# Performance work log

Measured on AMD Instinct MI355X. Metric: run time of the kernel, lower is better.

## Reference

```python
import jax, jax.numpy as jnp
import numpy as np

B, L = 256, 8192
ACF_PAD = L - 1          # acf_class[1]
POOL = 8                 # acf_class[2]
ACF_SIZE = ACF_PAD + 1   # == L, length kept after trim
POOLED = ACF_SIZE // POOL  # 1024, MLP input size
LIN = [512, 256]
OUT = 4                  # no_reg=False -> 4 outputs


def _linear_init(key, fan_out, fan_in):
    kw, kb = jax.random.split(key)
    bound = 1.0 / np.sqrt(fan_in)
    W = jax.random.uniform(kw, (fan_out, fan_in), jnp.float32, -bound, bound)
    b = jax.random.uniform(kb, (fan_out,), jnp.float32, -bound, bound)
    return W, b


def setup_inputs() -> dict:
    key = jax.random.key(0)
    kx, k1, k2, k3 = jax.random.split(key, 4)
    x = jax.random.normal(kx, (B, 1, L), jnp.float32)
    W1, b1 = _linear_init(k1, LIN[0], POOLED)
    W2, b2 = _linear_init(k2, LIN[1], LIN[0])
    W3, b3 = _linear_init(k3, OUT, LIN[1])
    return {"x": x, "W1": W1, "b1": b1, "W2": W2, "b2": b2, "W3": W3, "b3": b3}


def reference(x, W1, b1, W2, b2, W3, b3):
    # x: [B, 1, L]. Grouped conv1d with groups=B == per-sample autocorrelation.
    a = x[:, 0, :]                                             # [B, L]
    # full cross-correlation of a with itself: [B, 2L-1], lags -(L-1)..(L-1)
    corr = jax.vmap(lambda v: jnp.correlate(v, v, mode="full"))(a)
    # trim [:, acf_pad:] keeps non-negative lags 0..L-1 -> length ACF_SIZE
    r = corr[:, L - 1:]                                        # [B, L]
    # MaxPool1d(POOL), stride == POOL, floor division (L divisible here)
    pooled = r.reshape(B, POOLED, POOL).max(axis=-1)           # [B, POOLED]
    # normalize by per-sample max
    norm = pooled / jnp.max(pooled, axis=1, keepdims=True)
    # MLP: (Dropout is identity at inference) Linear -> LeakyReLU x2 -> Linear
    h = jax.nn.leaky_relu(norm @ W1.T + b1, negative_slope=0.01)
    h = jax.nn.leaky_relu(h @ W2.T + b2, negative_slope=0.01)
    return h @ W3.T + b3                                       # [B, 4]
```

## Files before the change

### kernel.cpp

```cpp
#include <hip/hip_runtime.h>

typedef __attribute__((ext_vector_type(8))) short bf16x8;
typedef __attribute__((ext_vector_type(16))) float f32x16;

#define LN 8192
#define SA_ROWB 4240
#define SB_OFF  33920
#define SMEM_BYTES 65536

__device__ __forceinline__ unsigned short f2bf(float f) {
    unsigned int u = __float_as_uint(f);
    u += 0x7fffu + ((u >> 16) & 1u);
    return (unsigned short)(u >> 16);
}
__device__ __forceinline__ float lrelu(float v) { return v > 0.f ? v : 0.01f * v; }
__device__ __forceinline__ float gldx(const float* p, int i) { return (i >= 0 && i < LN) ? p[i] : 0.f; }

__device__ __forceinline__ void dot8bf(uint4 q, const float* nl, float& acc) {
    acc += __uint_as_float(q.x << 16)          * nl[0];
    acc += __uint_as_float(q.x & 0xffff0000u)  * nl[1];
    acc += __uint_as_float(q.y << 16)          * nl[2];
    acc += __uint_as_float(q.y & 0xffff0000u)  * nl[3];
    acc += __uint_as_float(q.z << 16)          * nl[4];
    acc += __uint_as_float(q.z & 0xffff0000u)  * nl[5];
    acc += __uint_as_float(q.w << 16)          * nl[6];
    acc += __uint_as_float(q.w & 0xffff0000u)  * nl[7];
}

__global__ __launch_bounds__(512)
void conv_kernel(const float* __restrict__ W1, unsigned short* __restrict__ W1bf)
{
    const int idx = blockIdx.x * 512 + threadIdx.x;
    float4 v = ((const float4*)W1)[idx];
    ushort4 o;
    o.x = f2bf(v.x); o.y = f2bf(v.y); o.z = f2bf(v.z); o.w = f2bf(v.w);
    ((ushort4*)W1bf)[idx] = o;
}

__global__ __launch_bounds__(1024)
void fused_kernel(const float* __restrict__ x,
                  const unsigned short* __restrict__ W1bf, const float* __restrict__ b1,
                  const float* __restrict__ W2, const float* __restrict__ b2,
                  const float* __restrict__ W3, const float* __restrict__ b3,
                  float* __restrict__ out)
{
    __shared__ __align__(16) unsigned char smem[SMEM_BYTES];
    __shared__ float red[16];

    const int tid  = threadIdx.x;
    const int row  = blockIdx.x;
    const int lane = tid & 63;
    const int wv   = tid >> 6;
    const float* xr = x + (size_t)row * LN;

    const int jj = lane & 31;
    const int gp = lane >> 5;
    const int dd = lane & 7;
    const int hh = (lane >> 3) & 3;
    const int aoff_lane = dd * SA_ROWB + 64 + 16 * gp - 16 * hh;

    const int q  = wv & 3;
    const int p  = wv >> 2;
    const int T1 = p;
    const int T2 = 7 - p;
    const int s1 = 512 - 64 * p;
    const int s2 = 64 + 64 * p;

    for (int s = tid; s < 1156; s += 1024) {
        const int e0 = s * 8;
        float4 fa, fb;
        if (e0 + 7 < LN) {
            fa = *(const float4*)(xr + e0);
            fb = *(const float4*)(xr + e0 + 4);
        } else {
            fa = make_float4(gldx(xr,e0),   gldx(xr,e0+1), gldx(xr,e0+2), gldx(xr,e0+3));
            fb = make_float4(gldx(xr,e0+4), gldx(xr,e0+5), gldx(xr,e0+6), gldx(xr,e0+7));
        }
        uint4 pk;
        pk.x = (unsigned)f2bf(fa.x) | ((unsigned)f2bf(fa.y) << 16);
        pk.y = (unsigned)f2bf(fa.z) | ((unsigned)f2bf(fa.w) << 16);
        pk.z = (unsigned)f2bf(fb.x) | ((unsigned)f2bf(fb.y) << 16);
        pk.w = (unsigned)f2bf(fb.z) | ((unsigned)f2bf(fb.w) << 16);
        const int ph = s ^ ((s >> 3) & 7);
        *(uint4*)(smem + SB_OFF + ph * 16) = pk;
    }

    f32x16 acc1 = {}, acc2 = {};

    for (int ch = 0; ch < 4; ++ch) {
        const int tc = ch << 11;
        __syncthreads();
        if (tid < 528) {
            const int base = tc + 4 * tid - 40;
            float4 fa, fb, fc;
            if (base >= 0 && base + 11 < LN) {
                fa = *(const float4*)(xr + base);
                fb = *(const float4*)(xr + base + 4);
                fc = *(const float4*)(xr + base + 8);
            } else {
                fa = make_float4(gldx(xr,base),   gldx(xr,base+1), gldx(xr,base+2),  gldx(xr,base+3));
                fb = make_float4(gldx(xr,base+4), gldx(xr,base+5), gldx(xr,base+6),  gldx(xr,base+7));
                fc = make_float4(gldx(xr,base+8), gldx(xr,base+9), gldx(xr,base+10), gldx(xr,base+11));
            }
            unsigned short us[12];
            us[0]=f2bf(fa.x); us[1]=f2bf(fa.y); us[2]=f2bf(fa.z);  us[3]=f2bf(fa.w);
            us[4]=f2bf(fb.x); us[5]=f2bf(fb.y); us[6]=f2bf(fb.z);  us[7]=f2bf(fb.w);
            us[8]=f2bf(fc.x); us[9]=f2bf(fc.y); us[10]=f2bf(fc.z); us[11]=f2bf(fc.w);
            #pragma unroll
            for (int d = 0; d < 8; ++d) {
                unsigned long long pk = (unsigned long long)us[8-d]
                                      | ((unsigned long long)us[9-d]  << 16)
                                      | ((unsigned long long)us[10-d] << 32)
                                      | ((unsigned long long)us[11-d] << 48);
                *(unsigned long long*)(smem + d * SA_ROWB + 8 * tid) = pk;
            }
        }
        __syncthreads();

        const int c0 = ch * 128;
        int dD = s2 - c0; dD = dD < 0 ? 0 : (dD > 128 ? 128 : dD);
        int sLo = c0 > s2 ? c0 : s2;
        int sHi = (c0 + 128) < s1 ? (c0 + 128) : s1;
        int sS = sHi - sLo; if (sS < 0) sS = 0;
        const int wd0 = c0 + q * (dD >> 2),  wd1 = c0 + (q + 1) * (dD >> 2);
        const int ws0 = sLo + q * (sS >> 2), ws1 = sLo + (q + 1) * (sS >> 2);

        {
            const unsigned char* ap = smem + aoff_lane + 32 * (wd0 - c0);
            int S1 = 128 * T1 + 2 * wd0 + 4 * jj + gp;
            int S2 = 128 * T2 + 2 * wd0 + 4 * jj + gp;
            for (int mq = wd0; mq < wd1; mq += 4) {
                bf16x8 A[4], B1[4], B2[4];
                #pragma unroll
                for (int u = 0; u < 4; ++u) {
                    A[u] = *(const bf16x8*)(ap + 32 * u);
                    const int sa = S1 + 2 * u, sb = S2 + 2 * u;
                    B1[u] = *(const bf16x8*)(smem + SB_OFF + ((sa ^ ((sa >> 3) & 7)) << 4));
                    B2[u] = *(const bf16x8*)(smem + SB_OFF + ((sb ^ ((sb >> 3) & 7)) << 4));
                }
                #pragma unroll
                for (int u = 0; u < 4; ++u) {
                    acc1 = __builtin_amdgcn_mfma_f32_32x32x16_bf16(A[u], B1[u], acc1, 0, 0, 0);
                    acc2 = __builtin_amdgcn_mfma_f32_32x32x16_bf16(A[u], B2[u], acc2, 0, 0, 0);
                }
                ap += 128; S1 += 8; S2 += 8;
            }
        }
        {
            const unsigned char* ap = smem + aoff_lane + 32 * (ws0 - c0);
            int S1 = 128 * T1 + 2 * ws0 + 4 * jj + gp;
            for (int mq = ws0; mq < ws1; mq += 4) {
                bf16x8 A[4], B1[4];
                #pragma unroll
                for (int u = 0; u < 4; ++u) {
                    A[u] = *(const bf16x8*)(ap + 32 * u);
                    const int sa = S1 + 2 * u;
                    B1[u] = *(const bf16x8*)(smem + SB_OFF + ((sa ^ ((sa >> 3) & 7)) << 4));
                }
                #pragma unroll
                for (int u = 0; u < 4; ++u)
                    acc1 = __builtin_amdgcn_mfma_f32_32x32x16_bf16(A[u], B1[u], acc1, 0, 0, 0);
                ap += 128; S1 += 8;
            }
        }
    }

    __syncthreads();

    auto pwrite = [&](int T, int s, const f32x16& acc, bool add) {
        unsigned char* bp = smem + (T * 2 + s) * 4096 + jj * 128;
        #pragma unroll
        for (int rq = 0; rq < 4; ++rq) {
            const int bi = (2 * rq + gp) ^ (jj & 7);
            float4 w = make_float4(acc[4*rq], acc[4*rq+1], acc[4*rq+2], acc[4*rq+3]);
            float4* pp = (float4*)(bp + bi * 16);
            if (add) { float4 o = *pp; w.x += o.x; w.y += o.y; w.z += o.z; w.w += o.w; }
            *pp = w;
        }
    };
    if (q < 2) { pwrite(T1, q, acc1, false); pwrite(T2, q, acc2, false); }
    __syncthreads();
    if (q >= 2) { pwrite(T1, q - 2, acc1, true); pwrite(T2, q - 2, acc2, true); }
    __syncthreads();

    float* nrm = (float*)smem;
    float* h1  = (float*)(smem + 4096);
    float* h2  = (float*)(smem + 6144);
    {
        const int T  = tid >> 7;
        const int j2 = (tid >> 2) & 31;
        const int rq = tid & 3;
        const unsigned char* b0 = smem + (T * 2) * 4096 + j2 * 128;
        const int biA = (2 * rq)     ^ (j2 & 7);
        const int biB = (2 * rq + 1) ^ (j2 & 7);
        float4 s0a = *(const float4*)(b0 + biA * 16);
        float4 s0b = *(const float4*)(b0 + biB * 16);
        float4 s1a = *(const float4*)(b0 + 4096 + biA * 16);
        float4 s1b = *(const float4*)(b0 + 4096 + biB * 16);
        float v0 = s0a.x + s1a.x, v1 = s0a.y + s1a.y, v2 = s0a.z + s1a.z, v3 = s0a.w + s1a.w;
        float v4 = s0b.x + s1b.x, v5 = s0b.y + s1b.y, v6 = s0b.z + s1b.z, v7 = s0b.w + s1b.w;
        float m = fmaxf(fmaxf(fmaxf(v0, v1), fmaxf(v2, v3)), fmaxf(fmaxf(v4, v5), fmaxf(v6, v7)));

        float mx = m;
        for (int off = 32; off > 0; off >>= 1) mx = fmaxf(mx, __shfl_xor(mx, off));
        if (lane == 0) red[wv] = mx;
        __syncthreads();
        float pmax = red[0];
        #pragma unroll
        for (int k = 1; k < 16; ++k) pmax = fmaxf(pmax, red[k]);
        nrm[tid] = m * (1.0f / pmax);
    }
    __syncthreads();

    {
        float nlo[8], nhi[8];
        {
            const float4* n4 = (const float4*)nrm;
            float4 a0 = n4[2 * lane], a1 = n4[2 * lane + 1];
            float4 b0 = n4[128 + 2 * lane], b1v = n4[128 + 2 * lane + 1];
            nlo[0]=a0.x; nlo[1]=a0.y; nlo[2]=a0.z; nlo[3]=a0.w;
            nlo[4]=a1.x; nlo[5]=a1.y; nlo[6]=a1.z; nlo[7]=a1.w;
            nhi[0]=b0.x; nhi[1]=b0.y; nhi[2]=b0.z; nhi[3]=b0.w;
            nhi[4]=b1v.x; nhi[5]=b1v.y; nhi[6]=b1v.z; nhi[7]=b1v.w;
        }
        for (int n0 = 0; n0 < 32; n0 += 4) {
            const int nb = wv * 32 + n0;
            float s0 = 0.f, s1 = 0.f, s2v = 0.f, s3 = 0.f;
            {
                const uint4* r0 = (const uint4*)(W1bf + (size_t)nb * 1024);
                const uint4* r1 = (const uint4*)(W1bf + (size_t)(nb + 1) * 1024);
                const uint4* r2 = (const uint4*)(W1bf + (size_t)(nb + 2) * 1024);
                const uint4* r3 = (const uint4*)(W1bf + (size_t)(nb + 3) * 1024);
                uint4 qa0 = r0[lane], qb0 = r0[64 + lane];
                uint4 qa1 = r1[lane], qb1 = r1[64 + lane];
                uint4 qa2 = r2[lane], qb2 = r2[64 + lane];
                uint4 qa3 = r3[lane], qb3 = r3[64 + lane];
                dot8bf(qa0, nlo, s0); dot8bf(qb0, nhi, s0);
                dot8bf(qa1, nlo, s1); dot8bf(qb1, nhi, s1);
                dot8bf(qa2, nlo, s2v); dot8bf(qb2, nhi, s2v);
                dot8bf(qa3, nlo, s3); dot8bf(qb3, nhi, s3);
            }
            #pragma unroll
            for (int off = 32; off > 0; off >>= 1) {
                s0 += __shfl_xor(s0, off);
                s1 += __shfl_xor(s1, off);
                s2v += __shfl_xor(s2v, off);
                s3 += __shfl_xor(s3, off);
            }
            if (lane == 0) {
                h1[nb]     = lrelu(s0 + b1[nb]);
                h1[nb + 1] = lrelu(s1 + b1[nb + 1]);
                h1[nb + 2] = lrelu(s2v + b1[nb + 2]);
                h1[nb + 3] = lrelu(s3 + b1[nb + 3]);
            }
        }
    }
    __syncthreads();

    {
        const float4* a4 = (const float4*)h1;
        float4 av0 = a4[lane], av1 = a4[lane + 64];
        #pragma unroll
        for (int n0 = 0; n0 < 16; n0 += 8) {
            const int nb = wv * 16 + n0;
            float s[8];
            #pragma unroll
            for (int u = 0; u < 8; ++u) {
                const float4* wr = (const float4*)(W2 + (size_t)(nb + u) * 512);
                float4 w0 = wr[lane], w1 = wr[lane + 64];
                float t0 = w0.x*av0.x + w0.y*av0.y + w0.z*av0.z + w0.w*av0.w;
                float t1 = w1.x*av1.x + w1.y*av1.y + w1.z*av1.z + w1.w*av1.w;
                s[u] = t0 + t1;
            }
            #pragma unroll
            for (int off = 32; off > 0; off >>= 1) {
                #pragma unroll
                for (int u = 0; u < 8; ++u) s[u] += __shfl_xor(s[u], off);
            }
            if (lane == 0) {
                #pragma unroll
                for (int u = 0; u < 8; ++u) h2[nb + u] = lrelu(s[u] + b2[nb + u]);
            }
        }
    }
    __syncthreads();

    if (wv < 4) {
        const float4 w = ((const float4*)(W3 + wv * 256))[lane];
        const float4 a = ((const float4*)h2)[lane];
        float s = w.x*a.x + w.y*a.y + w.z*a.z + w.w*a.w;
        for (int off = 32; off > 0; off >>= 1) s += __shfl_xor(s, off);
        if (lane == 0) out[row * 4 + wv] = s + b3[wv];
    }
}

extern "C" void kernel_launch(void* const* d_in, const int* in_sizes, int n_in,
                              void* d_out, int out_size, void* d_ws, size_t ws_size,
                              hipStream_t stream)
{
    const float* x  = (const float*)d_in[0];
    const float* W1 = (const float*)d_in[1];
    const float* b1 = (const float*)d_in[2];
    const float* W2 = (const float*)d_in[3];
    const float* b2 = (const float*)d_in[4];
    const float* W3 = (const float*)d_in[5];
    const float* b3 = (const float*)d_in[6];
    float* outp = (float*)d_out;
    unsigned short* W1bf = (unsigned short*)d_ws;

    hipLaunchKernelGGL(conv_kernel,  dim3(256), dim3(512),  0, stream, W1, W1bf);
    hipLaunchKernelGGL(fused_kernel, dim3(256), dim3(1024), 0, stream,
                       x, W1bf, b1, W2, b2, W3, b3, outp);
}
```

Baseline: 49.84 us.

## Transpose and pack MLP weights for thread-per-output dot products without shuffles

The preprocessing kernel now converts W1 and also W2 to bf16 and stores them k-major, in 8-element packs interleaved across output neurons. In the MLP layers each thread then computes one output neuron over a slice of K, using coalesced weight loads and broadcast activation reads from shared memory. This replaces the per-warp cross-lane shuffle reductions with small shared-memory partial-sum combines. W2 now runs in bf16, which adds rounding error, and the layer-1 loop is longer per thread, which may expose load latency.

Result: faster. 45.48 us, median of 2 (-8.8%).

```diff
diff --git a/kernel.cpp b/kernel.cpp
--- a/kernel.cpp
+++ b/kernel.cpp
@@ -26,21 +26,37 @@
     acc += __uint_as_float(q.w << 16)          * nl[6];
     acc += __uint_as_float(q.w & 0xffff0000u)  * nl[7];
 }
-
-__global__ __launch_bounds__(512)
-void conv_kernel(const float* __restrict__ W1, unsigned short* __restrict__ W1bf)
+__device__ __forceinline__ uint4 pack8(float4 a, float4 b) {
+    uint4 pk;
+    pk.x = (unsigned)f2bf(a.x) | ((unsigned)f2bf(a.y) << 16);
+    pk.y = (unsigned)f2bf(a.z) | ((unsigned)f2bf(a.w) << 16);
+    pk.z = (unsigned)f2bf(b.x) | ((unsigned)f2bf(b.y) << 16);
+    pk.w = (unsigned)f2bf(b.z) | ((unsigned)f2bf(b.w) << 16);
+    return pk;
+}
+
+__global__ __launch_bounds__(256)
+void conv_kernel(const float* __restrict__ W1, const float* __restrict__ W2,
+                 uint4* __restrict__ W1p, uint4* __restrict__ W2p)
 {
-    const int idx = blockIdx.x * 512 + threadIdx.x;
-    float4 v = ((const float4*)W1)[idx];
-    ushort4 o;
-    o.x = f2bf(v.x); o.y = f2bf(v.y); o.z = f2bf(v.z); o.w = f2bf(v.w);
-    ((ushort4*)W1bf)[idx] = o;
+    const int b = blockIdx.x, t = threadIdx.x;
+    if (b < 256) {
+        const int g = b * 256 + t;
+        const int n = g >> 7, kqq = g & 127;
+        const float4* src = (const float4*)(W1 + (size_t)n * 1024 + 8 * kqq);
+        W1p[kqq * 512 + n] = pack8(src[0], src[1]);
+    } else {
+        const int g = (b - 256) * 256 + t;
+        const int n = g >> 6, kqq = g & 63;
+        const float4* src = (const float4*)(W2 + (size_t)n * 512 + 8 * kqq);
+        W2p[kqq * 256 + n] = pack8(src[0], src[1]);
+    }
 }
 
 __global__ __launch_bounds__(1024)
 void fused_kernel(const float* __restrict__ x,
-                  const unsigned short* __restrict__ W1bf, const float* __restrict__ b1,
-                  const float* __restrict__ W2, const float* __restrict__ b2,
+                  const uint4* __restrict__ W1p, const float* __restrict__ b1,
+                  const uint4* __restrict__ W2p, const float* __restrict__ b2,
                   const float* __restrict__ W3, const float* __restrict__ b3,
                   float* __restrict__ out)
 {
@@ -76,11 +92,7 @@
             fa = make_float4(gldx(xr,e0),   gldx(xr,e0+1), gldx(xr,e0+2), gldx(xr,e0+3));
             fb = make_float4(gldx(xr,e0+4), gldx(xr,e0+5), gldx(xr,e0+6), gldx(xr,e0+7));
         }
-        uint4 pk;
-        pk.x = (unsigned)f2bf(fa.x) | ((unsigned)f2bf(fa.y) << 16);
-        pk.y = (unsigned)f2bf(fa.z) | ((unsigned)f2bf(fa.w) << 16);
-        pk.z = (unsigned)f2bf(fb.x) | ((unsigned)f2bf(fb.y) << 16);
-        pk.w = (unsigned)f2bf(fb.z) | ((unsigned)f2bf(fb.w) << 16);
+        uint4 pk = pack8(fa, fb);
         const int ph = s ^ ((s >> 3) & 7);
         *(uint4*)(smem + SB_OFF + ph * 16) = pk;
     }
@@ -186,6 +198,9 @@
     float* nrm = (float*)smem;
     float* h1  = (float*)(smem + 4096);
     float* h2  = (float*)(smem + 6144);
+    float* ph  = (float*)(smem + 7168);
+    float* pe  = (float*)(smem + 9216);
+
     {
         const int T  = tid >> 7;
         const int j2 = (tid >> 2) & 31;
@@ -213,75 +228,42 @@
     __syncthreads();
 
     {
-        float nlo[8], nhi[8];
-        {
-            const float4* n4 = (const float4*)nrm;
-            float4 a0 = n4[2 * lane], a1 = n4[2 * lane + 1];
-            float4 b0 = n4[128 + 2 * lane], b1v = n4[128 + 2 * lane + 1];
-            nlo[0]=a0.x; nlo[1]=a0.y; nlo[2]=a0.z; nlo[3]=a0.w;
-            nlo[4]=a1.x; nlo[5]=a1.y; nlo[6]=a1.z; nlo[7]=a1.w;
-            nhi[0]=b0.x; nhi[1]=b0.y; nhi[2]=b0.z; nhi[3]=b0.w;
-            nhi[4]=b1v.x; nhi[5]=b1v.y; nhi[6]=b1v.z; nhi[7]=b1v.w;
-        }
-        for (int n0 = 0; n0 < 32; n0 += 4) {
-            const int nb = wv * 32 + n0;
-            float s0 = 0.f, s1 = 0.f, s2v = 0.f, s3 = 0.f;
-            {
-                const uint4* r0 = (const uint4*)(W1bf + (size_t)nb * 1024);
-                const uint4* r1 = (const uint4*)(W1bf + (size_t)(nb + 1) * 1024);
-                const uint4* r2 = (const uint4*)(W1bf + (size_t)(nb + 2) * 1024);
-                const uint4* r3 = (const uint4*)(W1bf + (size_t)(nb + 3) * 1024);
-                uint4 qa0 = r0[lane], qb0 = r0[64 + lane];
-                uint4 qa1 = r1[lane], qb1 = r1[64 + lane];
-                uint4 qa2 = r2[lane], qb2 = r2[64 + lane];
-                uint4 qa3 = r3[lane], qb3 = r3[64 + lane];
-                dot8bf(qa0, nlo, s0); dot8bf(qb0, nhi, s0);
-                dot8bf(qa1, nlo, s1); dot8bf(qb1, nhi, s1);
-                dot8bf(qa2, nlo, s2v); dot8bf(qb2, nhi, s2v);
-                dot8bf(qa3, nlo, s3); dot8bf(qb3, nhi, s3);
-            }
-            #pragma unroll
-            for (int off = 32; off > 0; off >>= 1) {
-                s0 += __shfl_xor(s0, off);
-                s1 += __shfl_xor(s1, off);
-                s2v += __shfl_xor(s2v, off);
-                s3 += __shfl_xor(s3, off);
-            }
-            if (lane == 0) {
-                h1[nb]     = lrelu(s0 + b1[nb]);
-                h1[nb + 1] = lrelu(s1 + b1[nb + 1]);
-                h1[nb + 2] = lrelu(s2v + b1[nb + 2]);
-                h1[nb + 3] = lrelu(s3 + b1[nb + 3]);
-            }
-        }
+        const int n  = tid & 511;
+        const int kh = tid >> 9;
+        const float4* n4 = (const float4*)nrm;
+        const uint4* wp = W1p + (size_t)kh * 64 * 512 + n;
+        float acc = 0.f;
+        #pragma unroll 8
+        for (int kq = 0; kq < 64; ++kq) {
+            uint4 qw = wp[kq * 512];
+            float4 a = n4[kh * 128 + 2 * kq];
+            float4 b = n4[kh * 128 + 2 * kq + 1];
+            float nl[8] = {a.x, a.y, a.z, a.w, b.x, b.y, b.z, b.w};
+            dot8bf(qw, nl, acc);
+        }
+        if (kh == 1) ph[n] = acc;
+        __syncthreads();
+        if (kh == 0) h1[n] = lrelu(acc + ph[n] + b1[n]);
     }
     __syncthreads();
 
     {
-        const float4* a4 = (const float4*)h1;
-        float4 av0 = a4[lane], av1 = a4[lane + 64];
+        const int n  = tid & 255;
+        const int qd = tid >> 8;
+        const float4* h4 = (const float4*)h1;
+        const uint4* wp = W2p + (size_t)qd * 16 * 256 + n;
+        float acc = 0.f;
         #pragma unroll
-        for (int n0 = 0; n0 < 16; n0 += 8) {
-            const int nb = wv * 16 + n0;
-            float s[8];
-            #pragma unroll
-            for (int u = 0; u < 8; ++u) {
-                const float4* wr = (const float4*)(W2 + (size_t)(nb + u) * 512);
-                float4 w0 = wr[lane], w1 = wr[lane + 64];
-                float t0 = w0.x*av0.x + w0.y*av0.y + w0.z*av0.z + w0.w*av0.w;
-                float t1 = w1.x*av1.x + w1.y*av1.y + w1.z*av1.z + w1.w*av1.w;
-                s[u] = t0 + t1;
-            }
-            #pragma unroll
-            for (int off = 32; off > 0; off >>= 1) {
-                #pragma unroll
-                for (int u = 0; u < 8; ++u) s[u] += __shfl_xor(s[u], off);
-            }
-            if (lane == 0) {
-                #pragma unroll
-                for (int u = 0; u < 8; ++u) h2[nb + u] = lrelu(s[u] + b2[nb + u]);
-            }
-        }
+        for (int kq = 0; kq < 16; ++kq) {
+            uint4 qw = wp[kq * 256];
+            float4 a = h4[qd * 32 + 2 * kq];
+            float4 b = h4[qd * 32 + 2 * kq + 1];
+            float nl[8] = {a.x, a.y, a.z, a.w, b.x, b.y, b.z, b.w};
+            dot8bf(qw, nl, acc);
+        }
+        if (qd > 0) pe[(qd - 1) * 256 + n] = acc;
+        __syncthreads();
+        if (qd == 0) h2[n] = lrelu(acc + pe[n] + pe[256 + n] + pe[512 + n] + b2[n]);
     }
     __syncthreads();
 
@@ -306,9 +288,10 @@
     const float* W3 = (const float*)d_in[5];
     const float* b3 = (const float*)d_in[6];
     float* outp = (float*)d_out;
-    unsigned short* W1bf = (unsigned short*)d_ws;
-
-    hipLaunchKernelGGL(conv_kernel,  dim3(256), dim3(512),  0, stream, W1, W1bf);
+    uint4* W1p = (uint4*)d_ws;
+    uint4* W2p = (uint4*)((char*)d_ws + (1 << 20));
+
+    hipLaunchKernelGGL(conv_kernel,  dim3(320), dim3(256),  0, stream, W1, W2, W1p, W2p);
     hipLaunchKernelGGL(fused_kernel, dim3(256), dim3(1024), 0, stream,
-                       x, W1bf, b1, W2, b2, W3, b3, outp);
-}
+                       x, W1p, b1, W2p, b2, W3, b3, outp);
+}
```
